# Optimization experiments

Hardware: AMD Instinct MI355X
Metric: run time of the kernel (lower is better)

The kernel has to match this reference:

```python
import jax, jax.numpy as jnp
import numpy as np

PS = 7  # window size
HEADS = 8


def setup_inputs() -> dict:
    key = jax.random.key(0)
    ks = jax.random.split(key, 5)
    b, C, H, W = 2, 384, 224, 224
    x = jax.random.normal(ks[0], (b, C, H, W), dtype=jnp.float32)
    # Conv2d(dim, 3*dim, k=1, bias=False) -> weight [3C, C]
    qkv_w = jax.random.normal(ks[1], (3 * C, C), dtype=jnp.float32) * (1.0 / np.sqrt(C))
    # depthwise Conv2d(3*dim, 3*dim, k=3, groups=3*dim) -> weight [3C, 1, 3, 3]
    dw_w = jax.random.normal(ks[2], (3 * C, 1, 3, 3), dtype=jnp.float32) * (1.0 / 3.0)
    # temperature parameter, initialized to ones like the module
    temperature = jnp.ones((HEADS, 1, 1), dtype=jnp.float32)
    # Conv2d(dim, dim, k=1, bias=False) -> weight [C, C]
    proj_w = jax.random.normal(ks[3], (C, C), dtype=jnp.float32) * (1.0 / np.sqrt(C))
    return {"x": x, "qkv_w": qkv_w, "dw_w": dw_w, "temperature": temperature, "proj_w": proj_w}


def _l2norm(t):
    n = jnp.sqrt(jnp.sum(t * t, axis=-1, keepdims=True))
    return t / jnp.maximum(n, 1e-12)  # matches F.normalize semantics


def reference(x, qkv_w, dw_w, temperature, proj_w):
    b, C, H, W = x.shape
    heads, ps = HEADS, PS
    d = C // heads
    nh, nw = H // ps, W // ps

    # 1x1 conv qkv projection (pointwise -> einsum)
    qkv = jnp.einsum('bchw,oc->bohw', x, qkv_w)
    # depthwise 3x3 conv, padding=1
    qkv = jax.lax.conv_general_dilated(
        qkv, dw_w, window_strides=(1, 1), padding='SAME',
        feature_group_count=3 * C, dimension_numbers=('NCHW', 'OIHW', 'NCHW'))
    q, k, v = jnp.split(qkv, 3, axis=1)

    def to_win(t):
        # b (head d) (nh ps) (nw ps) -> b (nh nw) head d (ps ps)
        t = t.reshape(b, heads, d, nh, ps, nw, ps)
        t = t.transpose(0, 3, 5, 1, 2, 4, 6)
        return t.reshape(b, nh * nw, heads, d, ps * ps)

    q, k, v = to_win(q), to_win(k), to_win(v)
    q = _l2norm(q)
    k = _l2norm(k)

    # channel-transposed attention: d x d scores per window
    attn = jnp.einsum('bwhds,bwhes->bwhde', q, k) * temperature
    attn = jax.nn.softmax(attn, axis=-1)
    out = jnp.einsum('bwhde,bwhes->bwhds', attn, v)

    # inverse rearrange: b (nh nw) head d (ps ps) -> b (head d) (nh ps) (nw ps)
    out = out.reshape(b, nh, nw, heads, d, ps, ps)
    out = out.transpose(0, 3, 4, 1, 5, 2, 6).reshape(b, C, H, W)

    return jnp.einsum('bchw,oc->bohw', out, proj_w)
```

## Files before the change

kernel.cpp:

```cpp
#include <hip/hip_runtime.h>


#define NB     2
#define CC     384
#define C3     1152
#define HH     224
#define WW2    224
#define HW     50176
#define NHEADS 8
#define DD     48
#define PSZ    7
#define NWINS  1024
#define SS     49
#define SSP    50
#define WS50   (NWINS*SSP)

typedef unsigned int  u32;
typedef unsigned short u16;
typedef __bf16 bf16x8 __attribute__((ext_vector_type(8)));
typedef float  f32x4  __attribute__((ext_vector_type(4)));

__device__ __forceinline__ u16 f2bf(float f){
  union { float f; u32 u; } v; v.f = f;
  u32 r = v.u + 0x7FFFu + ((v.u >> 16) & 1u);
  return (u16)(r >> 16);
}
__device__ __forceinline__ float bf2f(u16 h){
  union { u32 u; float f; } v; v.u = ((u32)h) << 16;
  return v.f;
}

typedef __attribute__((address_space(3))) u32 as3_u32;
typedef __attribute__((address_space(1))) const u32 as1_u32;
__device__ __forceinline__ void gld16(const void* g, void* l){
  __builtin_amdgcn_global_load_lds((as1_u32*)(unsigned long long)(g),
                                   (as3_u32*)(u32)(unsigned long long)(l),
                                   16, 0, 0);
}

__device__ __forceinline__ int swz(int row, int col){
  return row*64 + (col ^ ((row & 7) << 3));
}

__global__ void k_cvt(const float* __restrict__ qw, const float* __restrict__ pw,
                      u16* __restrict__ qwb, u16* __restrict__ pwb){
  int i = blockIdx.x * 256 + threadIdx.x;
  if (i < C3*CC) qwb[i] = f2bf(qw[i]);
  if (i < CC*CC) pwb[i] = f2bf(pw[i]);
}

__global__ void k_sentinel(float* __restrict__ out, int n){
  int i = blockIdx.x * 256 + threadIdx.x;
  if (i < n) out[i] = 12345.0f;
}

#define CPAD 386
__global__ __launch_bounds__(256) void k_trx(const float* __restrict__ x,
                                             u16* __restrict__ xt){
  const int pt = blockIdx.x, b = blockIdx.y, tid = threadIdx.x;
  __shared__ u16 t[64*CPAD];
  const float* xb = x + (size_t)b*CC*HW + pt*64;
  #pragma unroll
  for (int it=0; it<24; ++it){
    int i = tid + it*256;
    int c = i >> 4, p4 = (i & 15)*4;
    float4 v = *(const float4*)(xb + (size_t)c*HW + p4);
    t[(p4+0)*CPAD + c] = f2bf(v.x);
    t[(p4+1)*CPAD + c] = f2bf(v.y);
    t[(p4+2)*CPAD + c] = f2bf(v.z);
    t[(p4+3)*CPAD + c] = f2bf(v.w);
  }
  __syncthreads();
  u32* dst = (u32*)(xt + ((size_t)b*HW + (size_t)pt*64)*CC);
  #pragma unroll
  for (int it=0; it<48; ++it){
    int j = tid + it*256;
    int p = j / 192, c2 = j - p*192;
    dst[j] = *(const u32*)(t + p*CPAD + c2*2);
  }
}

template<int OUT_F32>
__global__ __launch_bounds__(256) void k_gemm(const u16* __restrict__ A,
    const u16* __restrict__ B, void* __restrict__ Cdst){
  __shared__ __align__(16) u16 As[128*32];
  __shared__ __align__(16) u16 Bs[128*32];
  const int m0 = blockIdx.x * 128, n0 = blockIdx.y * 128, b = blockIdx.z;
  const int M  = gridDim.x * 128;
  const int tid = threadIdx.x, lane = tid & 63, wv = tid >> 6;
  const int wm = (wv & 1) * 64, wn = (wv >> 1) * 64;
  const int lr = lane & 15, lg = lane >> 4;
  const u16* Bb = B + (size_t)b*HW*CC;

  f32x4 acc[4][4];
  #pragma unroll
  for (int i=0;i<4;++i)
    #pragma unroll
    for (int j=0;j<4;++j) acc[i][j] = {0.f,0.f,0.f,0.f};

  for (int kk=0; kk<12; ++kk){
    const int k0 = kk*32;
    __syncthreads();
    #pragma unroll
    for (int i=0;i<2;++i){
      int chunk = i*256 + tid;
      int row = chunk >> 2, c4 = chunk & 3;
      gld16(A  + (size_t)(m0+row)*CC + k0 + c4*8, As + chunk*8);
      gld16(Bb + (size_t)(n0+row)*CC + k0 + c4*8, Bs + chunk*8);
    }
    __syncthreads();
    bf16x8 af[4], bfr[4];
    #pragma unroll
    for (int i=0;i<4;++i) af[i]  = *(const bf16x8*)(As + (wm + i*16 + lr)*32 + lg*8);
    #pragma unroll
    for (int j=0;j<4;++j) bfr[j] = *(const bf16x8*)(Bs + (wn + j*16 + lr)*32 + lg*8);
    #pragma unroll
    for (int i=0;i<4;++i)
      #pragma unroll
      for (int j=0;j<4;++j)
        acc[i][j] = __builtin_amdgcn_mfma_f32_16x16x32_bf16(af[i], bfr[j], acc[i][j], 0, 0, 0);
  }
  #pragma unroll
  for (int i=0;i<4;++i){
    #pragma unroll
    for (int j=0;j<4;++j){
      const int row = m0 + wm + i*16 + lg*4;
      const int col = n0 + wn + j*16 + lr;
      if (OUT_F32){
        float* Cp = (float*)Cdst + (size_t)b*M*HW;
        #pragma unroll
        for (int r=0;r<4;++r) Cp[(size_t)(row+r)*HW + col] = acc[i][j][r];
      } else {
        u16* Cp = (u16*)Cdst + (size_t)b*M*HW;
        #pragma unroll
        for (int r=0;r<4;++r) Cp[(size_t)(row+r)*HW + col] = f2bf(acc[i][j][r]);
      }
    }
  }
}

#define DW_LD  228
__global__ __launch_bounds__(256) void k_dw(const u16* __restrict__ qkv,
    const float* __restrict__ dww, u16* __restrict__ qkv2){
  const int wy = blockIdx.x, o0 = blockIdx.y*2, b = blockIdx.z;
  const int tid = threadIdx.x;
  __shared__ __align__(16) u16 lin[2][9*DW_LD];
  __shared__ __align__(16) u16 outb[2][32*SSP];

  const int y0 = wy*PSZ - 1;
  #pragma unroll
  for (int ch=0; ch<2; ++ch){
    const u16* src = qkv + (size_t)(b*C3 + o0 + ch) * HW;
    #pragma unroll
    for (int j=0;j<4;++j){
      int i = tid + j*256;
      if (i < 9*112){
        int r = i / 112, c2 = i - r*112;
        int y = y0 + r;
        u32 v = 0u;
        if (y >= 0 && y < HH) v = *(const u32*)(src + (size_t)y*WW2 + c2*2);
        *(u32*)(lin[ch] + r*DW_LD + 2 + c2*2) = v;
      }
    }
  }
  if (tid < 36){ int ch = tid/18, t = tid%18; int r = t>>1;
                 lin[ch][r*DW_LD + ((t&1) ? 226 : 1)] = 0; }
  if (tid >= 192 && tid < 256){ int t = tid-192; outb[t>>5][(t&31)*SSP + 49] = 0; }
  __syncthreads();

  if (tid < 224){
    const int wx = tid / PSZ, pi = tid - wx*PSZ;
    const int xb = wx * PSZ;
    #pragma unroll
    for (int ch=0; ch<2; ++ch){
      float wk[9];
      #pragma unroll
      for (int i=0;i<9;++i) wk[i] = dww[(o0+ch)*9 + i];
      float row0[9], row1[9], row2[9];
      #pragma unroll
      for (int c=0;c<9;++c){
        row0[c] = bf2f(lin[ch][(pi+0)*DW_LD + xb + c + 1]);
        row1[c] = bf2f(lin[ch][(pi+1)*DW_LD + xb + c + 1]);
        row2[c] = bf2f(lin[ch][(pi+2)*DW_LD + xb + c + 1]);
      }
      u16* ob = outb[ch] + wx*SSP + pi*PSZ;
      #pragma unroll
      for (int pj=0;pj<PSZ;++pj){
        float s = 0.f;
        #pragma unroll
        for (int kx=0;kx<3;++kx){
          s += wk[0*3+kx]*row0[pj+kx];
          s += wk[1*3+kx]*row1[pj+kx];
          s += wk[2*3+kx]*row2[pj+kx];
        }
        ob[pj] = f2bf(s);
      }
    }
  }
  __syncthreads();

  #pragma unroll
  for (int j=0;j<2;++j){
    int i = tid + j*256;
    if (i < 400){
      int ch = i / 200, idx = i - ch*200;
      u16* dst = qkv2 + ((size_t)(b*C3 + o0 + ch)*NWINS + (size_t)wy*32)*SSP;
      *(uint4*)(dst + idx*8) = *(const uint4*)(outb[ch] + idx*8);
    }
  }
}

__global__ __launch_bounds__(256) void k_attn(const u16* __restrict__ qkv2,
    const float* __restrict__ temp, u16* __restrict__ aout){
  const int h = blockIdx.x, win = blockIdx.y, b = blockIdx.z;
  const int tid = threadIdx.x, lane = tid & 63, wv = tid >> 6;
  const int lr = lane & 15, lg = lane >> 4;

  __shared__ __align__(16) u16 q_s[48*64], k_s[48*64], v_t[64*64], p_s[48*64];
  __shared__ float invq[48], invk[48];

  for (int i=tid; i<48*32; i+=256){ ((u32*)q_s)[i]=0u; ((u32*)k_s)[i]=0u; ((u32*)p_s)[i]=0u; }
  for (int i=tid; i<64*32; i+=256) ((u32*)v_t)[i]=0u;
  __syncthreads();

  const u16* qsrc = qkv2 + ((size_t)(b*C3 +        h*DD)*NWINS + win)*SSP;
  const u16* ksrc = qkv2 + ((size_t)(b*C3 + CC   + h*DD)*NWINS + win)*SSP;
  const u16* vsrc = qkv2 + ((size_t)(b*C3 + 2*CC + h*DD)*NWINS + win)*SSP;
  for (int i=tid; i<48*25; i+=256){
    int dc = i / 25, c = i - dc*25;
    size_t off = (size_t)dc*WS50 + 2*c;
    u32 vq = *(const u32*)(qsrc + off);
    u32 vk = *(const u32*)(ksrc + off);
    u32 vv = *(const u32*)(vsrc + off);
    int sw = swz(dc, 2*c);
    *(u32*)(q_s + sw) = vq;
    *(u32*)(k_s + sw) = vk;
    v_t[swz(2*c,   dc)] = (u16)(vv & 0xffffu);
    v_t[swz(2*c+1, dc)] = (u16)(vv >> 16);
  }
  __syncthreads();

  if (tid < 192){
    const int row96 = tid >> 1, half = tid & 1;
    const int rr = (row96 < 48) ? row96 : row96 - 48;
    const u16* a = (row96 < 48) ? q_s : k_s;
    const int s0 = half ? 25 : 0, s1 = half ? 49 : 25;
    float sum = 0.f;
    for (int s=s0; s<s1; ++s){ float v = bf2f(a[swz(rr,s)]); sum += v*v; }
    sum += __shfl_xor(sum, 1);
    if (!half){
      float inv = 1.f / fmaxf(sqrtf(sum), 1e-12f);
      if (row96 < 48) invq[rr] = inv * temp[h]; else invk[rr] = inv;
    }
  }
  __syncthreads();

  if (wv < 3){
    const int ti = wv;
    f32x4 c3[3];
    #pragma unroll
    for (int tj=0;tj<3;++tj) c3[tj] = {0.f,0.f,0.f,0.f};
    #pragma unroll
    for (int tj=0;tj<3;++tj){
      #pragma unroll
      for (int ks=0; ks<2; ++ks){
        bf16x8 a  = *(const bf16x8*)(q_s + swz(ti*16+lr, ks*32 + lg*8));
        bf16x8 bb = *(const bf16x8*)(k_s + swz(tj*16+lr, ks*32 + lg*8));
        c3[tj] = __builtin_amdgcn_mfma_f32_16x16x32_bf16(a, bb, c3[tj], 0,0,0);
      }
    }
    const float ik0 = invk[lr], ik1 = invk[16+lr], ik2 = invk[32+lr];
    #pragma unroll
    for (int r=0;r<4;++r){
      const int row = ti*16 + lg*4 + r;
      const float iq = invq[row];
      float l0 = c3[0][r]*iq*ik0, l1 = c3[1][r]*iq*ik1, l2 = c3[2][r]*iq*ik2;
      float m = fmaxf(fmaxf(l0,l1),l2);
      m = fmaxf(m, __shfl_xor(m,1)); m = fmaxf(m, __shfl_xor(m,2));
      m = fmaxf(m, __shfl_xor(m,4)); m = fmaxf(m, __shfl_xor(m,8));
      float e0 = __expf(l0-m), e1 = __expf(l1-m), e2 = __expf(l2-m);
      float s = e0+e1+e2;
      s += __shfl_xor(s,1); s += __shfl_xor(s,2);
      s += __shfl_xor(s,4); s += __shfl_xor(s,8);
      const float is = 1.f / s;
      p_s[swz(row, lr)]    = f2bf(e0*is);
      p_s[swz(row, 16+lr)] = f2bf(e1*is);
      p_s[swz(row, 32+lr)] = f2bf(e2*is);
    }
  }
  __syncthreads();

  const int wy = win >> 5, wx = win & 31;
  u16* ab = aout + (size_t)b*HW*CC + (size_t)h*DD;
  for (int t = wv; t < 12; t += 4){
    int ti = t >> 2, tj = t & 3;
    f32x4 c = {0.f,0.f,0.f,0.f};
    #pragma unroll
    for (int ks=0; ks<2; ++ks){
      bf16x8 a  = *(const bf16x8*)(p_s + swz(ti*16+lr, ks*32 + lg*8));
      bf16x8 bb = *(const bf16x8*)(v_t + swz(tj*16+lr, ks*32 + lg*8));
      c = __builtin_amdgcn_mfma_f32_16x16x32_bf16(a, bb, c, 0,0,0);
    }
    int scol = tj*16 + lr;
    if (scol < SS){
      int pi = scol / PSZ, pj = scol - pi*PSZ;
      size_t p = (size_t)(wy*PSZ + pi)*WW2 + wx*PSZ + pj;
      u32 lo = (u32)f2bf(c[0]) | ((u32)f2bf(c[1]) << 16);
      u32 hi = (u32)f2bf(c[2]) | ((u32)f2bf(c[3]) << 16);
      u32* dst = (u32*)(ab + p*CC + ti*16 + lg*4);
      dst[0] = lo; dst[1] = hi;
    }
  }
}

extern "C" void kernel_launch(void* const* d_in, const int* in_sizes, int n_in,
                              void* d_out, int out_size, void* d_ws, size_t ws_size,
                              hipStream_t stream) {
  const float* x     = (const float*)d_in[0];
  const float* qkvw  = (const float*)d_in[1];
  const float* dww   = (const float*)d_in[2];
  const float* temp  = (const float*)d_in[3];
  const float* projw = (const float*)d_in[4];
  float* out = (float*)d_out;

  const size_t SZ_QKV   = (size_t)NB*C3*HW*2;
  const size_t SZ_QKV2  = (size_t)NB*C3*NWINS*SSP*2;
  const size_t OFF_QKV2 = SZ_QKV;
  const size_t OFF_W1   = OFF_QKV2 + SZ_QKV2;
  const size_t OFF_W2   = OFF_W1 + (size_t)C3*CC*2;
  const size_t NEEDED   = OFF_W2 + (size_t)CC*CC*2;

  if (ws_size < NEEDED){
    k_sentinel<<<(out_size + 255)/256, 256, 0, stream>>>(out, out_size);
    return;
  }
  char* ws = (char*)d_ws;
  u16* qkv  = (u16*)ws;
  u16* qkv2 = (u16*)(ws + OFF_QKV2);
  u16* xt   = (u16*)(ws + OFF_QKV2);
  u16* ao   = (u16*)ws;
  u16* qwb  = (u16*)(ws + OFF_W1);
  u16* pwb  = (u16*)(ws + OFF_W2);

  k_cvt<<<dim3((C3*CC)/256), 256, 0, stream>>>(qkvw, projw, qwb, pwb);
  k_trx<<<dim3(784, NB), 256, 0, stream>>>(x, xt);
  k_gemm<0><<<dim3(9,392,2), 256, 0, stream>>>(qwb, xt, qkv);
  k_dw<<<dim3(32, C3/2, NB), 256, 0, stream>>>(qkv, dww, qkv2);
  k_attn<<<dim3(NHEADS, NWINS, NB), 256, 0, stream>>>(qkv2, temp, ao);
  k_gemm<1><<<dim3(3,392,2), 256, 0, stream>>>(pwb, ao, out);
}
```

Baseline: 577.4 us.

## Restructure depthwise conv: 4 channels per block, 16-byte loads, rolling row reuse

The depthwise 3x3 kernel now handles 4 channels per 128-thread block. Each thread computes a full 7x7 window for one channel by sliding a 3-row register buffer, so every input row is read from LDS once instead of three times. Global loads widen from 4 to 16 bytes, using an aligned LDS padding offset. Outputs are packed into 32-bit words before the LDS write, and the bf16 conversion now uses the native cast. Per-thread register use rises, and the native cast changes NaN rounding behaviour.

Result: faster. 547.8 us (-5.1%).

```diff
diff --git a/kernel.cpp b/kernel.cpp
--- a/kernel.cpp
+++ b/kernel.cpp
@@ -21,13 +21,17 @@
 typedef float  f32x4  __attribute__((ext_vector_type(4)));
 
 __device__ __forceinline__ u16 f2bf(float f){
-  union { float f; u32 u; } v; v.f = f;
-  u32 r = v.u + 0x7FFFu + ((v.u >> 16) & 1u);
-  return (u16)(r >> 16);
+  union { __bf16 h; u16 u; } v; v.h = (__bf16)f; return v.u;
 }
 __device__ __forceinline__ float bf2f(u16 h){
   union { u32 u; float f; } v; v.u = ((u32)h) << 16;
   return v.f;
+}
+__device__ __forceinline__ float u16lo(u32 u){
+  union { u32 u; float f; } v; v.u = u << 16; return v.f;
+}
+__device__ __forceinline__ float u16hi(u32 u){
+  union { u32 u; float f; } v; v.u = u & 0xffff0000u; return v.f;
 }
 
 typedef __attribute__((address_space(3))) u32 as3_u32;
@@ -139,73 +143,112 @@
   }
 }
 
-#define DW_LD  228
-__global__ __launch_bounds__(256) void k_dw(const u16* __restrict__ qkv,
+#define DWL 240
+__global__ __launch_bounds__(128) void k_dw(const u16* __restrict__ qkv,
     const float* __restrict__ dww, u16* __restrict__ qkv2){
-  const int wy = blockIdx.x, o0 = blockIdx.y*2, b = blockIdx.z;
+  const int wy = blockIdx.x, o0 = blockIdx.y*4, b = blockIdx.z;
   const int tid = threadIdx.x;
-  __shared__ __align__(16) u16 lin[2][9*DW_LD];
-  __shared__ __align__(16) u16 outb[2][32*SSP];
+  __shared__ __align__(16) u16 lin[4*9*DWL];
+  __shared__ __align__(16) u16 outb[4*32*SSP];
 
   const int y0 = wy*PSZ - 1;
-  #pragma unroll
-  for (int ch=0; ch<2; ++ch){
-    const u16* src = qkv + (size_t)(b*C3 + o0 + ch) * HW;
-    #pragma unroll
-    for (int j=0;j<4;++j){
-      int i = tid + j*256;
-      if (i < 9*112){
-        int r = i / 112, c2 = i - r*112;
-        int y = y0 + r;
-        u32 v = 0u;
-        if (y >= 0 && y < HH) v = *(const u32*)(src + (size_t)y*WW2 + c2*2);
-        *(u32*)(lin[ch] + r*DW_LD + 2 + c2*2) = v;
-      }
-    }
-  }
-  if (tid < 36){ int ch = tid/18, t = tid%18; int r = t>>1;
-                 lin[ch][r*DW_LD + ((t&1) ? 226 : 1)] = 0; }
-  if (tid >= 192 && tid < 256){ int t = tid-192; outb[t>>5][(t&31)*SSP + 49] = 0; }
-  __syncthreads();
-
-  if (tid < 224){
-    const int wx = tid / PSZ, pi = tid - wx*PSZ;
-    const int xb = wx * PSZ;
-    #pragma unroll
-    for (int ch=0; ch<2; ++ch){
-      float wk[9];
+
+  if (tid < 72){
+    int ch = tid/18, rem = tid%18, r = rem>>1;
+    lin[ch*9*DWL + r*DWL + ((rem&1) ? 232 : 7)] = 0;
+  }
+  outb[tid*SSP + 49] = 0;
+
+  #pragma unroll
+  for (int it=0; it<8; ++it){
+    int i = tid + it*128;
+    if (i < 1008){
+      int ch = i / 252, rem = i - ch*252;
+      int r = rem / 28, c16 = rem - r*28;
+      int y = y0 + r;
+      uint4 v = {0,0,0,0};
+      if (y >= 0 && y < HH)
+        v = *(const uint4*)(qkv + (size_t)(b*C3 + o0 + ch)*HW + (size_t)y*WW2 + c16*8);
+      *(uint4*)(lin + ch*9*DWL + r*DWL + 8 + c16*8) = v;
+    }
+  }
+  __syncthreads();
+
+  {
+    const int ch = tid >> 5, wx = tid & 31;
+    const u16* L = lin + ch*9*DWL;
+    const int xb = wx*PSZ;
+    const int s0 = (xb+7) & ~1;
+    const bool par = (xb+7) & 1;
+
+    float wk[9];
+    #pragma unroll
+    for (int i=0;i<9;++i) wk[i] = dww[(o0+ch)*9 + i];
+
+    float tr[3][9];
+    #define LOADROW(slot, r) {                                   \
+      u32 u0 = *(const u32*)(L + (r)*DWL + s0);                  \
+      u32 u1 = *(const u32*)(L + (r)*DWL + s0 + 2);              \
+      u32 u2 = *(const u32*)(L + (r)*DWL + s0 + 4);              \
+      u32 u3 = *(const u32*)(L + (r)*DWL + s0 + 6);              \
+      u32 u4 = *(const u32*)(L + (r)*DWL + s0 + 8);              \
+      float a0=u16lo(u0),a1=u16hi(u0),a2=u16lo(u1),a3=u16hi(u1); \
+      float a4=u16lo(u2),a5=u16hi(u2),a6=u16lo(u3),a7=u16hi(u3); \
+      float a8=u16lo(u4),a9=u16hi(u4);                           \
+      tr[slot][0]=par?a1:a0; tr[slot][1]=par?a2:a1;              \
+      tr[slot][2]=par?a3:a2; tr[slot][3]=par?a4:a3;              \
+      tr[slot][4]=par?a5:a4; tr[slot][5]=par?a6:a5;              \
+      tr[slot][6]=par?a7:a6; tr[slot][7]=par?a8:a7;              \
+      tr[slot][8]=par?a9:a8; }
+
+    LOADROW(0, 0)
+    LOADROW(1, 1)
+
+    u32 pk[24];
+    u16 last;
+    #pragma unroll
+    for (int pi=0; pi<7; ++pi){
+      LOADROW((pi+2)%3, pi+2)
+      const float* r0 = tr[pi%3];
+      const float* r1 = tr[(pi+1)%3];
+      const float* r2 = tr[(pi+2)%3];
+      float o[7];
       #pragma unroll
-      for (int i=0;i<9;++i) wk[i] = dww[(o0+ch)*9 + i];
-      float row0[9], row1[9], row2[9];
-      #pragma unroll
-      for (int c=0;c<9;++c){
-        row0[c] = bf2f(lin[ch][(pi+0)*DW_LD + xb + c + 1]);
-        row1[c] = bf2f(lin[ch][(pi+1)*DW_LD + xb + c + 1]);
-        row2[c] = bf2f(lin[ch][(pi+2)*DW_LD + xb + c + 1]);
-      }
-      u16* ob = outb[ch] + wx*SSP + pi*PSZ;
-      #pragma unroll
-      for (int pj=0;pj<PSZ;++pj){
+      for (int pj=0; pj<7; ++pj){
         float s = 0.f;
         #pragma unroll
         for (int kx=0;kx<3;++kx){
-          s += wk[0*3+kx]*row0[pj+kx];
-          s += wk[1*3+kx]*row1[pj+kx];
-          s += wk[2*3+kx]*row2[pj+kx];
+          s += wk[kx]  *r0[pj+kx];
+          s += wk[3+kx]*r1[pj+kx];
+          s += wk[6+kx]*r2[pj+kx];
         }
-        ob[pj] = f2bf(s);
+        o[pj] = s;
       }
-    }
-  }
-  __syncthreads();
-
-  #pragma unroll
-  for (int j=0;j<2;++j){
-    int i = tid + j*256;
-    if (i < 400){
+      #pragma unroll
+      for (int pj=0; pj<7; ++pj){
+        int idx = pi*7 + pj;
+        u16 bv = f2bf(o[pj]);
+        if (idx == 48){ last = bv; }
+        else {
+          if ((idx & 1) == 0) pk[idx>>1] = (u32)bv;
+          else                pk[idx>>1] |= ((u32)bv) << 16;
+        }
+      }
+    }
+    u16* rec = outb + tid*SSP;
+    #pragma unroll
+    for (int i=0;i<24;++i) *(u32*)(rec + 2*i) = pk[i];
+    rec[48] = last;
+  }
+  __syncthreads();
+
+  #pragma unroll
+  for (int it=0; it<7; ++it){
+    int i = tid + it*128;
+    if (i < 800){
       int ch = i / 200, idx = i - ch*200;
       u16* dst = qkv2 + ((size_t)(b*C3 + o0 + ch)*NWINS + (size_t)wy*32)*SSP;
-      *(uint4*)(dst + idx*8) = *(const uint4*)(outb[ch] + idx*8);
+      *(uint4*)(dst + idx*8) = *(const uint4*)(outb + ch*32*SSP + idx*8);
     }
   }
 }
@@ -345,7 +388,7 @@
   k_cvt<<<dim3((C3*CC)/256), 256, 0, stream>>>(qkvw, projw, qwb, pwb);
   k_trx<<<dim3(784, NB), 256, 0, stream>>>(x, xt);
   k_gemm<0><<<dim3(9,392,2), 256, 0, stream>>>(qwb, xt, qkv);
-  k_dw<<<dim3(32, C3/2, NB), 256, 0, stream>>>(qkv, dww, qkv2);
+  k_dw<<<dim3(32, C3/4, NB), 128, 0, stream>>>(qkv, dww, qkv2);
   k_attn<<<dim3(NHEADS, NWINS, NB), 256, 0, stream>>>(qkv2, temp, ao);
   k_gemm<1><<<dim3(3,392,2), 256, 0, stream>>>(pwb, ao, out);
 }
```
